# Kernel tuning notes

Hardware: AMD Instinct MI355X
Metric: run time of the kernel (lower is better)

The kernel has to match this reference:

```python
import jax, jax.numpy as jnp
import numpy as np


def _deform_conv2d(x, offset, weight, stride=(1, 1), pad=(1, 1), dilation=(1, 1)):
    # x: [B,C,H,W]; offset: [B, 2*Goff*kh*kw, oh, ow]; weight: [OC, C//Gw, kh, kw]
    B, C, H, W = x.shape
    OC, Cg, kh, kw = weight.shape
    Gw = C // Cg
    K = kh * kw
    sh, sw = stride
    ph, pw = pad
    dh, dw = dilation
    oh = (H + 2 * ph - (dh * (kh - 1) + 1)) // sh + 1
    ow = (W + 2 * pw - (dw * (kw - 1) + 1)) // sw + 1
    Goff = offset.shape[1] // (2 * K)
    # torchvision layout: per offset group, per kernel tap k, (dy, dx)
    off = offset.reshape(B, Goff, K, 2, oh, ow)
    ki = jnp.arange(K) // kw  # kernel row per tap
    kj = jnp.arange(K) % kw   # kernel col per tap
    base_y = jnp.arange(oh) * sh - ph
    base_x = jnp.arange(ow) * sw - pw
    gy = (base_y[None, :] + (ki * dh)[:, None]).astype(x.dtype)  # [K, oh]
    gx = (base_x[None, :] + (kj * dw)[:, None]).astype(x.dtype)  # [K, ow]
    py = off[:, :, :, 0] + gy[None, None, :, :, None]  # [B,Goff,K,oh,ow]
    px = off[:, :, :, 1] + gx[None, None, :, None, :]
    cpg = C // Goff  # channels per offset group
    py = jnp.repeat(py, cpg, axis=1)  # [B,C,K,oh,ow]
    px = jnp.repeat(px, cpg, axis=1)
    xf = x.reshape(B, C, H * W)
    y0 = jnp.floor(py)
    x0 = jnp.floor(px)
    ty = py - y0
    tx = px - x0
    y0i = y0.astype(jnp.int32)
    x0i = x0.astype(jnp.int32)

    def gather(cy, cx):
        valid = (cy >= 0) & (cy < H) & (cx >= 0) & (cx < W)
        idx = jnp.clip(cy, 0, H - 1) * W + jnp.clip(cx, 0, W - 1)
        v = jnp.take_along_axis(xf, idx.reshape(B, C, -1), axis=2).reshape(idx.shape)
        return jnp.where(valid, v, jnp.zeros((), x.dtype))

    # bilinear sample, zero padding outside image (matches torchvision)
    v = (gather(y0i, x0i) * (1 - ty) * (1 - tx)
         + gather(y0i, x0i + 1) * (1 - ty) * tx
         + gather(y0i + 1, x0i) * ty * (1 - tx)
         + gather(y0i + 1, x0i + 1) * ty * tx)  # [B,C,K,oh,ow]
    v = v.reshape(B, Gw, Cg, K, oh, ow)
    wg = weight.reshape(Gw, OC // Gw, Cg, K)
    out = jnp.einsum('bgckhw,gock->bgohw', v, wg)
    return out.reshape(B, OC, oh, ow)


def setup_inputs() -> dict:
    key = jax.random.key(0)
    k1, k2, k3 = jax.random.split(key, 3)
    x = jax.random.normal(k1, (8, 64, 56, 56), dtype=jnp.float32)
    offset = jax.random.normal(k2, (8, 18, 56, 56), dtype=jnp.float32)
    weight = jax.random.normal(k3, (64, 64, 3, 3), dtype=jnp.float32) * 0.05
    return {"input": x, "offset": offset, "weight": weight}


def reference(input, offset, weight):
    return _deform_conv2d(input, offset, weight, stride=(1, 1), pad=(1, 1), dilation=(1, 1))
```

## Files before the change

kernel.cpp:

```cpp
#include <hip/hip_runtime.h>
#include <hip/hip_fp16.h>


typedef _Float16 f16x8 __attribute__((ext_vector_type(8)));
typedef float    f32x4 __attribute__((ext_vector_type(4)));

namespace {
constexpr int Bn = 8, Cn = 64, Hn = 56, Wn = 56;
constexpr int Kk = 9, OCn = 64;
constexpr int NPIX = 56 * 56;
constexpr int CK   = Cn * Kk;
constexpr int TP   = 32;
constexpr int TILES = NPIX / TP;
constexpr int XTILES = NPIX / 64;
constexpr int KSTEPS = CK / 32;
}

__device__ __forceinline__ __half2 u2h(unsigned u) {
    union { unsigned u; __half2 h; } x; x.u = u; return x.h;
}
__device__ __forceinline__ unsigned bcast_h(float f) {
    unsigned short hs = __half_as_ushort(__float2half(f));
    return (unsigned)hs * 0x10001u;
}
__device__ __forceinline__ void lds_barrier() {
    asm volatile("s_waitcnt lgkmcnt(0)" ::: "memory");
    __builtin_amdgcn_s_barrier();
}
__device__ __forceinline__ void gld16(uint4& d, const unsigned short* p) {
    asm volatile("global_load_dwordx4 %0, %1, off" : "=&v"(d) : "v"(p) : "memory");
}

__global__ __launch_bounds__(256) void prep_kernel(
    const float* __restrict__ x, const float* __restrict__ w,
    unsigned short* __restrict__ xh, unsigned short* __restrict__ wh2)
{
    const int tid = threadIdx.x;
    if (blockIdx.x >= 392) {
        const int i = (blockIdx.x - 392) * 256 + tid;
        if (i < OCn * CK) {
            const int j    = i & 7;
            const int lane = (i >> 3) & 63;
            const int rest = i >> 9;
            const int og   = rest / KSTEPS;
            const int oc   = og * 16 + (lane & 15);
            const int kglob = (rest % KSTEPS) * 32 + (lane >> 4) * 8 + j;
            const int tap = kglob >> 6;
            const int c   = kglob & 63;
            wh2[i] = __half_as_ushort(__float2half(w[oc * CK + c * Kk + tap]));
        }
        return;
    }
    __shared__ unsigned short lds[64][66];
    const int b  = blockIdx.x / XTILES;
    const int t0 = (blockIdx.x % XTILES) * 64;
    const float* xb = x + (size_t)b * Cn * NPIX;
    {
        const int hw0 = (tid & 15) * 4;
        #pragma unroll
        for (int i = 0; i < 4; ++i) {
            const int c = (tid >> 4) + i * 16;
            const float4 v = *(const float4*)(xb + (size_t)c * NPIX + t0 + hw0);
            lds[hw0 + 0][c] = __half_as_ushort(__float2half(v.x));
            lds[hw0 + 1][c] = __half_as_ushort(__float2half(v.y));
            lds[hw0 + 2][c] = __half_as_ushort(__float2half(v.z));
            lds[hw0 + 3][c] = __half_as_ushort(__float2half(v.w));
        }
    }
    __syncthreads();
    {
        const int co = (tid & 7) * 8;
        #pragma unroll
        for (int i = 0; i < 2; ++i) {
            const int hw = (tid >> 3) + i * 32;
            unsigned short tmp[8] __attribute__((aligned(16)));
            #pragma unroll
            for (int j = 0; j < 8; ++j) tmp[j] = lds[hw][co + j];
            *(uint4*)(xh + ((size_t)b * NPIX + t0 + hw) * Cn + co) = *(const uint4*)tmp;
        }
    }
}

__global__ __launch_bounds__(128, 3) void deform_fused(
    const unsigned short* __restrict__ xh, const float* __restrict__ off,
    const unsigned short* __restrict__ wh2, float* __restrict__ out)
{
    __shared__ uint4 smpw[Kk * TP];
    __shared__ int4  smpa[Kk * TP];
    __shared__ __align__(16) uint4 vbuf[3][8 * TP];

    const int tid = threadIdx.x;
    const int b  = blockIdx.x / TILES;
    const int p0 = (blockIdx.x % TILES) * TP;
    const unsigned short* xb = xh + (size_t)b * NPIX * Cn;
    const float* offb = off + (size_t)b * 18 * NPIX;

    for (int e = tid; e < Kk * TP; e += 128) {
        const int k  = e >> 5;
        const int px = e & 31;
        const int p  = p0 + px;
        const int oy = p / Wn, ox = p % Wn;
        const int ki = k / 3, kj = k % 3;
        const float offy = offb[(size_t)(2 * k)     * NPIX + p];
        const float offx = offb[(size_t)(2 * k + 1) * NPIX + p];
        const float py  = offy + (float)(oy - 1 + ki);
        const float pxv = offx + (float)(ox - 1 + kj);
        const float y0f = floorf(py), x0f = floorf(pxv);
        const float ty = py - y0f, tx = pxv - x0f;
        const int y0 = (int)y0f, x0 = (int)x0f;
        const int y1 = y0 + 1, x1 = x0 + 1;
        const bool vy0 = (y0 >= 0) & (y0 < Hn);
        const bool vy1 = (y1 >= 0) & (y1 < Hn);
        const bool vx0 = (x0 >= 0) & (x0 < Wn);
        const bool vx1 = (x1 >= 0) & (x1 < Wn);
        const int cy0 = min(max(y0, 0), Hn - 1);
        const int cy1 = min(max(y1, 0), Hn - 1);
        const int cx0 = min(max(x0, 0), Wn - 1);
        const int cx1 = min(max(x1, 0), Wn - 1);
        uint4 wq;
        wq.x = bcast_h((vy0 && vx0) ? (1.f - ty) * (1.f - tx) : 0.f);
        wq.y = bcast_h((vy0 && vx1) ? (1.f - ty) * tx         : 0.f);
        wq.z = bcast_h((vy1 && vx0) ? ty * (1.f - tx)         : 0.f);
        wq.w = bcast_h((vy1 && vx1) ? ty * tx                 : 0.f);
        int4 av;
        av.x = (cy0 * Wn + cx0) * Cn;
        av.y = (cy0 * Wn + cx1) * Cn;
        av.z = (cy1 * Wn + cx0) * Cn;
        av.w = (cy1 * Wn + cx1) * Cn;
        smpw[e] = wq;
        smpa[e] = av;
    }
    lds_barrier();
    asm volatile("s_waitcnt vmcnt(0)" ::: "memory");

    const int oct  = tid & 7;
    const int gpx0 = (tid >> 3) & 15;
    const int co   = oct * 8;

    const int lane = tid & 63;
    const int wv   = tid >> 6;
    const int hi   = lane >> 4;
    const int lr   = lane & 15;
    const uint4* ab0 = (const uint4*)wh2 + (size_t)(wv * 2 + 0) * KSTEPS * 64 + lane;
    const uint4* ab1 = (const uint4*)wh2 + (size_t)(wv * 2 + 1) * KSTEPS * 64 + lane;

    uint4 s0[2][2], s1[2][2], s2[2][2], s3[2][2], wqr[2][2];
    uint4 aF[2][2][2];
    f32x4 acc[2][2] = {{{0.f,0.f,0.f,0.f},{0.f,0.f,0.f,0.f}},
                       {{0.f,0.f,0.f,0.f},{0.f,0.f,0.f,0.f}}};

    auto stageC = [&](int k) {
        const int sl = k & 1;
        #pragma unroll
        for (int u = 0; u < 2; ++u) {
            const int m  = k * TP + gpx0 + u * 16;
            const int4 av = smpa[m];
            wqr[sl][u] = smpw[m];
            gld16(s0[sl][u], xb + av.x + co);
            gld16(s1[sl][u], xb + av.y + co);
            gld16(s2[sl][u], xb + av.z + co);
            gld16(s3[sl][u], xb + av.w + co);
        }
    };
    auto loadA = [&](int k) {
        const int sl = k & 1;
        gld16(aF[sl][0][0], (const unsigned short*)(ab0 + (k * 2 + 0) * 64));
        gld16(aF[sl][0][1], (const unsigned short*)(ab0 + (k * 2 + 1) * 64));
        gld16(aF[sl][1][0], (const unsigned short*)(ab1 + (k * 2 + 0) * 64));
        gld16(aF[sl][1][1], (const unsigned short*)(ab1 + (k * 2 + 1) * 64));
    };
    auto blend = [&](int k) {
        const int sl = k & 1;
        #pragma unroll
        for (int u = 0; u < 2; ++u) {
            const __half2 w00 = u2h(wqr[sl][u].x), w01 = u2h(wqr[sl][u].y);
            const __half2 w10 = u2h(wqr[sl][u].z), w11 = u2h(wqr[sl][u].w);
            uint4 res;
            unsigned* rp = (unsigned*)&res;
            #pragma unroll
            for (int q = 0; q < 4; ++q) {
                __half2 a = __hmul2(w00, u2h(((const unsigned*)&s0[sl][u])[q]));
                a = __hfma2(w01, u2h(((const unsigned*)&s1[sl][u])[q]), a);
                a = __hfma2(w10, u2h(((const unsigned*)&s2[sl][u])[q]), a);
                a = __hfma2(w11, u2h(((const unsigned*)&s3[sl][u])[q]), a);
                rp[q] = *(const unsigned*)&a;
            }
            vbuf[k % 3][oct * TP + gpx0 + u * 16] = res;
        }
    };
    auto mfma = [&](int k) {
        const int sl = k % 3;
        #pragma unroll
        for (int kl = 0; kl < 2; ++kl) {
            const int octr = kl * 4 + hi;
            union { uint4 u; f16x8 h; } b0, b1;
            b0.u = vbuf[sl][octr * TP + lr];
            b1.u = vbuf[sl][octr * TP + 16 + lr];
            #pragma unroll
            for (int ogi = 0; ogi < 2; ++ogi) {
                union { uint4 u; f16x8 h; } a;
                a.u = aF[k & 1][ogi][kl];
                acc[ogi][0] = __builtin_amdgcn_mfma_f32_16x16x32_f16(a.h, b0.h, acc[ogi][0], 0, 0, 0);
                acc[ogi][1] = __builtin_amdgcn_mfma_f32_16x16x32_f16(a.h, b1.h, acc[ogi][1], 0, 0, 0);
            }
        }
    };

    stageC(0); stageC(1);
    loadA(0);
    asm volatile("s_waitcnt vmcnt(12)" ::: "memory");
    __builtin_amdgcn_sched_barrier(0);
    blend(0);
    lds_barrier();

    #pragma unroll
    for (int k = 0; k < Kk; ++k) {
        if (k < Kk - 2) stageC(k + 2);
        if (k < Kk - 1) loadA(k + 1);
        if (k < Kk - 2)       asm volatile("s_waitcnt vmcnt(12)" ::: "memory");
        else if (k == Kk - 2) asm volatile("s_waitcnt vmcnt(4)"  ::: "memory");
        else                  asm volatile("s_waitcnt vmcnt(0)"  ::: "memory");
        __builtin_amdgcn_sched_barrier(0);
        if (k < Kk - 1) blend(k + 1);
        mfma(k);
        lds_barrier();
    }

    #pragma unroll
    for (int ogi = 0; ogi < 2; ++ogi) {
        float* ob = out + ((size_t)b * OCn + (wv * 2 + ogi) * 16 + hi * 4) * NPIX + p0 + lr;
        #pragma unroll
        for (int r = 0; r < 4; ++r) {
            ob[(size_t)r * NPIX]      = acc[ogi][0][r];
            ob[(size_t)r * NPIX + 16] = acc[ogi][1][r];
        }
    }
}

extern "C" void kernel_launch(void* const* d_in, const int* in_sizes, int n_in,
                              void* d_out, int out_size, void* d_ws, size_t ws_size,
                              hipStream_t stream) {
    const float* x   = (const float*)d_in[0];
    const float* off = (const float*)d_in[1];
    const float* w   = (const float*)d_in[2];
    float* out = (float*)d_out;
    unsigned short* wh2 = (unsigned short*)d_ws;
    unsigned short* xh  = (unsigned short*)((char*)d_ws + 131072);

    hipLaunchKernelGGL(prep_kernel, dim3(392 + 144), dim3(256), 0, stream, x, w, xh, wh2);
    hipLaunchKernelGGL(deform_fused, dim3(Bn * TILES), dim3(128), 0, stream,
                       xh, off, wh2, out);
}
```

Baseline: 22.18 us.

## Double pixel tile to 64 with 256-thread blocks, one OC group per wave

Doubles the pixel tile per block from 32 to 64 and grows blocks to 256 threads with four waves. Each wave now owns one 16-channel output group across four pixel subtiles instead of two output groups across two subtiles. The blended sample tile in LDS is now shared by four waves, and each wave loads half as many weight fragments. Block indexing is also interleaved by batch (blockIdx & 7) in both kernels, which spreads consecutive blocks across images. The grid halves to 392 blocks and per-block LDS grows, which may reduce occupancy and the number of blocks available per CU.

After: 21.60 us. 2.6% less time.

```diff
diff --git a/kernel.cpp b/kernel.cpp
--- a/kernel.cpp
+++ b/kernel.cpp
@@ -10,7 +10,7 @@
 constexpr int Kk = 9, OCn = 64;
 constexpr int NPIX = 56 * 56;
 constexpr int CK   = Cn * Kk;
-constexpr int TP   = 32;
+constexpr int TP   = 64;
 constexpr int TILES = NPIX / TP;
 constexpr int XTILES = NPIX / 64;
 constexpr int KSTEPS = CK / 32;
@@ -52,8 +52,8 @@
         return;
     }
     __shared__ unsigned short lds[64][66];
-    const int b  = blockIdx.x / XTILES;
-    const int t0 = (blockIdx.x % XTILES) * 64;
+    const int b  = blockIdx.x & 7;
+    const int t0 = (blockIdx.x >> 3) * 64;
     const float* xb = x + (size_t)b * Cn * NPIX;
     {
         const int hw0 = (tid & 15) * 4;
@@ -81,7 +81,7 @@
     }
 }
 
-__global__ __launch_bounds__(128, 3) void deform_fused(
+__global__ __launch_bounds__(256, 3) void deform_fused(
     const unsigned short* __restrict__ xh, const float* __restrict__ off,
     const unsigned short* __restrict__ wh2, float* __restrict__ out)
 {
@@ -90,14 +90,14 @@
     __shared__ __align__(16) uint4 vbuf[3][8 * TP];
 
     const int tid = threadIdx.x;
-    const int b  = blockIdx.x / TILES;
-    const int p0 = (blockIdx.x % TILES) * TP;
+    const int b  = blockIdx.x & 7;
+    const int p0 = (blockIdx.x >> 3) * TP;
     const unsigned short* xb = xh + (size_t)b * NPIX * Cn;
     const float* offb = off + (size_t)b * 18 * NPIX;
 
-    for (int e = tid; e < Kk * TP; e += 128) {
-        const int k  = e >> 5;
-        const int px = e & 31;
+    for (int e = tid; e < Kk * TP; e += 256) {
+        const int k  = e >> 6;
+        const int px = e & 63;
         const int p  = p0 + px;
         const int oy = p / Wn, ox = p % Wn;
         const int ki = k / 3, kj = k % 3;
@@ -134,26 +134,25 @@
     asm volatile("s_waitcnt vmcnt(0)" ::: "memory");
 
     const int oct  = tid & 7;
-    const int gpx0 = (tid >> 3) & 15;
+    const int gpx0 = (tid >> 3) & 31;
     const int co   = oct * 8;
 
     const int lane = tid & 63;
-    const int wv   = tid >> 6;
+    const int og   = tid >> 6;
     const int hi   = lane >> 4;
     const int lr   = lane & 15;
-    const uint4* ab0 = (const uint4*)wh2 + (size_t)(wv * 2 + 0) * KSTEPS * 64 + lane;
-    const uint4* ab1 = (const uint4*)wh2 + (size_t)(wv * 2 + 1) * KSTEPS * 64 + lane;
+    const uint4* ab = (const uint4*)wh2 + (size_t)og * KSTEPS * 64 + lane;
 
     uint4 s0[2][2], s1[2][2], s2[2][2], s3[2][2], wqr[2][2];
-    uint4 aF[2][2][2];
-    f32x4 acc[2][2] = {{{0.f,0.f,0.f,0.f},{0.f,0.f,0.f,0.f}},
-                       {{0.f,0.f,0.f,0.f},{0.f,0.f,0.f,0.f}}};
+    uint4 aF[2][2];
+    f32x4 acc[4] = {{0.f,0.f,0.f,0.f},{0.f,0.f,0.f,0.f},
+                    {0.f,0.f,0.f,0.f},{0.f,0.f,0.f,0.f}};
 
     auto stageC = [&](int k) {
         const int sl = k & 1;
         #pragma unroll
         for (int u = 0; u < 2; ++u) {
-            const int m  = k * TP + gpx0 + u * 16;
+            const int m  = k * TP + gpx0 + u * 32;
             const int4 av = smpa[m];
             wqr[sl][u] = smpw[m];
             gld16(s0[sl][u], xb + av.x + co);
@@ -164,10 +163,8 @@
     };
     auto loadA = [&](int k) {
         const int sl = k & 1;
-        gld16(aF[sl][0][0], (const unsigned short*)(ab0 + (k * 2 + 0) * 64));
-        gld16(aF[sl][0][1], (const unsigned short*)(ab0 + (k * 2 + 1) * 64));
-        gld16(aF[sl][1][0], (const unsigned short*)(ab1 + (k * 2 + 0) * 64));
-        gld16(aF[sl][1][1], (const unsigned short*)(ab1 + (k * 2 + 1) * 64));
+        gld16(aF[sl][0], (const unsigned short*)(ab + (k * 2 + 0) * 64));
+        gld16(aF[sl][1], (const unsigned short*)(ab + (k * 2 + 1) * 64));
     };
     auto blend = [&](int k) {
         const int sl = k & 1;
@@ -185,7 +182,7 @@
                 a = __hfma2(w11, u2h(((const unsigned*)&s3[sl][u])[q]), a);
                 rp[q] = *(const unsigned*)&a;
             }
-            vbuf[k % 3][oct * TP + gpx0 + u * 16] = res;
+            vbuf[k % 3][oct * TP + gpx0 + u * 32] = res;
         }
     };
     auto mfma = [&](int k) {
@@ -193,22 +190,20 @@
         #pragma unroll
         for (int kl = 0; kl < 2; ++kl) {
             const int octr = kl * 4 + hi;
-            union { uint4 u; f16x8 h; } b0, b1;
-            b0.u = vbuf[sl][octr * TP + lr];
-            b1.u = vbuf[sl][octr * TP + 16 + lr];
+            union { uint4 u; f16x8 h; } a;
+            a.u = aF[k & 1][kl];
             #pragma unroll
-            for (int ogi = 0; ogi < 2; ++ogi) {
-                union { uint4 u; f16x8 h; } a;
-                a.u = aF[k & 1][ogi][kl];
-                acc[ogi][0] = __builtin_amdgcn_mfma_f32_16x16x32_f16(a.h, b0.h, acc[ogi][0], 0, 0, 0);
-                acc[ogi][1] = __builtin_amdgcn_mfma_f32_16x16x32_f16(a.h, b1.h, acc[ogi][1], 0, 0, 0);
+            for (int ct = 0; ct < 4; ++ct) {
+                union { uint4 u; f16x8 h; } bb;
+                bb.u = vbuf[sl][octr * TP + ct * 16 + lr];
+                acc[ct] = __builtin_amdgcn_mfma_f32_16x16x32_f16(a.h, bb.h, acc[ct], 0, 0, 0);
             }
         }
     };
 
     stageC(0); stageC(1);
     loadA(0);
-    asm volatile("s_waitcnt vmcnt(12)" ::: "memory");
+    asm volatile("s_waitcnt vmcnt(10)" ::: "memory");
     __builtin_amdgcn_sched_barrier(0);
     blend(0);
     lds_barrier();
@@ -217,8 +212,8 @@
     for (int k = 0; k < Kk; ++k) {
         if (k < Kk - 2) stageC(k + 2);
         if (k < Kk - 1) loadA(k + 1);
-        if (k < Kk - 2)       asm volatile("s_waitcnt vmcnt(12)" ::: "memory");
-        else if (k == Kk - 2) asm volatile("s_waitcnt vmcnt(4)"  ::: "memory");
+        if (k < Kk - 2)       asm volatile("s_waitcnt vmcnt(10)" ::: "memory");
+        else if (k == Kk - 2) asm volatile("s_waitcnt vmcnt(2)"  ::: "memory");
         else                  asm volatile("s_waitcnt vmcnt(0)"  ::: "memory");
         __builtin_amdgcn_sched_barrier(0);
         if (k < Kk - 1) blend(k + 1);
@@ -227,13 +222,10 @@
     }
 
     #pragma unroll
-    for (int ogi = 0; ogi < 2; ++ogi) {
-        float* ob = out + ((size_t)b * OCn + (wv * 2 + ogi) * 16 + hi * 4) * NPIX + p0 + lr;
-        #pragma unroll
-        for (int r = 0; r < 4; ++r) {
-            ob[(size_t)r * NPIX]      = acc[ogi][0][r];
-            ob[(size_t)r * NPIX + 16] = acc[ogi][1][r];
-        }
+    for (int ct = 0; ct < 4; ++ct) {
+        float* ob = out + ((size_t)b * OCn + og * 16 + hi * 4) * NPIX + p0 + ct * 16 + lr;
+        #pragma unroll
+        for (int r = 0; r < 4; ++r) ob[(size_t)r * NPIX] = acc[ct][r];
     }
 }
 
@@ -248,6 +240,6 @@
     unsigned short* xh  = (unsigned short*)((char*)d_ws + 131072);
 
     hipLaunchKernelGGL(prep_kernel, dim3(392 + 144), dim3(256), 0, stream, x, w, xh, wh2);
-    hipLaunchKernelGGL(deform_fused, dim3(Bn * TILES), dim3(128), 0, stream,
+    hipLaunchKernelGGL(deform_fused, dim3(Bn * TILES), dim3(256), 0, stream,
                        xh, off, wh2, out);
 }
```
